# Kernel tuning notes

Measured on AMD Instinct MI355X. Metric: run time of the kernel, lower is better.

The kernel has to match this reference:

```python
import jax, jax.numpy as jnp
import numpy as np

B, S, D, H = 2, 2048, 1024, 16
DH = D // H
DFF = 4 * D
EPS = 1e-5


def layernorm(x, g, b):
    mu = jnp.mean(x, axis=-1, keepdims=True)
    var = jnp.mean(jnp.square(x - mu), axis=-1, keepdims=True)
    return (x - mu) * jax.lax.rsqrt(var + EPS) * g + b


def setup_inputs() -> dict:
    key = jax.random.key(0)
    ks = jax.random.split(key, 12)
    s = 0.02
    return {
        "x": jax.random.normal(ks[0], (B, S, D), dtype=jnp.float32),
        "ln1_g": jnp.ones((D,), jnp.float32),
        "ln1_b": jnp.zeros((D,), jnp.float32),
        "Wq": jax.random.normal(ks[1], (D, D), jnp.float32) * s,
        "bq": jnp.zeros((D,), jnp.float32),
        "Wk": jax.random.normal(ks[2], (D, D), jnp.float32) * s,
        "bk": jnp.zeros((D,), jnp.float32),
        "Wv": jax.random.normal(ks[3], (D, D), jnp.float32) * s,
        "bv": jnp.zeros((D,), jnp.float32),
        "Wo": jax.random.normal(ks[4], (D, D), jnp.float32) * s,
        "bo": jnp.zeros((D,), jnp.float32),
        "ln2_g": jnp.ones((D,), jnp.float32),
        "ln2_b": jnp.zeros((D,), jnp.float32),
        "W1": jax.random.normal(ks[5], (D, DFF), jnp.float32) * s,
        "b1": jnp.zeros((DFF,), jnp.float32),
        "W2": jax.random.normal(ks[6], (DFF, D), jnp.float32) * s,
        "b2": jnp.zeros((D,), jnp.float32),
    }


def block(x, ln1_g, ln1_b, Wq, bq, Wk, bk, Wv, bv, Wo, bo, ln2_g, ln2_b, W1, b1, W2, b2):
    h = layernorm(x, ln1_g, ln1_b)
    # projections -> [B, H, S, DH]
    q = (h @ Wq + bq).reshape(B, S, H, DH).transpose(0, 2, 1, 3)
    k = (h @ Wk + bk).reshape(B, S, H, DH).transpose(0, 2, 1, 3)
    v = (h @ Wv + bv).reshape(B, S, H, DH).transpose(0, 2, 1, 3)
    scores = jnp.einsum('bhqd,bhkd->bhqk', q, k) / jnp.sqrt(jnp.float32(DH))
    causal = jnp.tril(jnp.ones((S, S), dtype=bool))  # True = keep
    scores = jnp.where(causal, scores, -jnp.inf)
    attn = jax.nn.softmax(scores, axis=-1)
    out = jnp.einsum('bhqk,bhkd->bhqd', attn, v)
    out = out.transpose(0, 2, 1, 3).reshape(B, S, D)
    x = x + out @ Wo + bo
    h2 = layernorm(x, ln2_g, ln2_b)
    ff = jax.nn.gelu(h2 @ W1 + b1, approximate=False) @ W2 + b2
    return x + ff


def reference(x, ln1_g, ln1_b, Wq, bq, Wk, bk, Wv, bv, Wo, bo, ln2_g, ln2_b, W1, b1, W2, b2):
    return block(x, ln1_g, ln1_b, Wq, bq, Wk, bk, Wv, bv, Wo, bo, ln2_g, ln2_b, W1, b1, W2, b2)
```

## Files before the change

### kernel.cpp

```cpp
#include <hip/hip_runtime.h>
#include <cstdint>
#include <cstddef>


#define DEV static __device__ __forceinline__

typedef unsigned short u16;
typedef __bf16 bf16x8 __attribute__((ext_vector_type(8)));
typedef u16    u16x8  __attribute__((ext_vector_type(8)));
typedef u16    u16x4  __attribute__((ext_vector_type(4)));
typedef float  f32x4  __attribute__((ext_vector_type(4)));

#define AEXP2(x) __builtin_amdgcn_exp2f(x)

DEV u16 f2bf(float f) {
  unsigned u = __builtin_bit_cast(unsigned, f);
  u += 0x7fffu + ((u >> 16) & 1u);
  return (u16)(u >> 16);
}

DEV void gl16(const void* g, void* l) {
  __builtin_amdgcn_global_load_lds(
      (const __attribute__((address_space(1))) unsigned*)g,
      (__attribute__((address_space(3))) unsigned*)l, 16, 0, 0);
}

__global__ __launch_bounds__(256)
void tconv(const float* __restrict__ in, u16* __restrict__ out, int R, int C)
{
  __shared__ float tile[32][33];
  const int tx = threadIdx.x & 31, ty = threadIdx.x >> 5;
  const int r0 = blockIdx.y * 32, c0 = blockIdx.x * 32;
#pragma unroll
  for (int i = 0; i < 4; ++i)
    tile[ty + 8*i][tx] = in[(size_t)(r0 + ty + 8*i) * C + c0 + tx];
  __syncthreads();
#pragma unroll
  for (int i = 0; i < 4; ++i)
    out[(size_t)(c0 + ty + 8*i) * R + r0 + tx] = f2bf(tile[tx][ty + 8*i]);
}

__global__ __launch_bounds__(256)
void tconv4(const float* __restrict__ w0, const float* __restrict__ w1,
            const float* __restrict__ w2, const float* __restrict__ w3,
            u16* __restrict__ q0, u16* __restrict__ q1,
            u16* __restrict__ q2, u16* __restrict__ q3)
{
  __shared__ float tile[32][33];
  const int z = blockIdx.z;
  const float* in = z == 0 ? w0 : z == 1 ? w1 : z == 2 ? w2 : w3;
  u16* out       = z == 0 ? q0 : z == 1 ? q1 : z == 2 ? q2 : q3;
  const int tx = threadIdx.x & 31, ty = threadIdx.x >> 5;
  const int r0 = blockIdx.y * 32, c0 = blockIdx.x * 32;
#pragma unroll
  for (int i = 0; i < 4; ++i)
    tile[ty + 8*i][tx] = in[(size_t)(r0 + ty + 8*i) * 1024 + c0 + tx];
  __syncthreads();
#pragma unroll
  for (int i = 0; i < 4; ++i)
    out[(size_t)(c0 + ty + 8*i) * 1024 + r0 + tx] = f2bf(tile[tx][ty + 8*i]);
}

__global__ __launch_bounds__(256)
void ln_fwd(const float* __restrict__ x, const float* __restrict__ g,
            const float* __restrict__ b, u16* __restrict__ out)
{
  const int row = blockIdx.x, t = threadIdx.x;
  const float4 v = ((const float4*)(x + (size_t)row * 1024))[t];
  float s1 = v.x + v.y + v.z + v.w;
  float s2 = v.x*v.x + v.y*v.y + v.z*v.z + v.w*v.w;
#pragma unroll
  for (int d = 1; d < 64; d <<= 1) {
    s1 += __shfl_xor(s1, d, 64);
    s2 += __shfl_xor(s2, d, 64);
  }
  __shared__ float sh[8];
  const int w = t >> 6;
  if ((t & 63) == 0) { sh[w] = s1; sh[w + 4] = s2; }
  __syncthreads();
  s1 = sh[0] + sh[1] + sh[2] + sh[3];
  s2 = sh[4] + sh[5] + sh[6] + sh[7];
  const float mu  = s1 * (1.0f / 1024.0f);
  const float var = s2 * (1.0f / 1024.0f) - mu * mu;
  const float rs  = rsqrtf(var + 1e-5f);
  const float4 gv = ((const float4*)g)[t];
  const float4 bv = ((const float4*)b)[t];
  u16x4 o;
  o[0] = f2bf((v.x - mu) * rs * gv.x + bv.x);
  o[1] = f2bf((v.y - mu) * rs * gv.y + bv.y);
  o[2] = f2bf((v.z - mu) * rs * gv.z + bv.z);
  o[3] = f2bf((v.w - mu) * rs * gv.w + bv.w);
  *(u16x4*)(out + (size_t)row * 1024 + t * 4) = o;
}

#define EPI_QKV  0
#define EPI_RES  1
#define EPI_GELU 2

#define QSCALE 0.180421f

template<int EPI, int BM>
__global__ __launch_bounds__(256)
void gemm_bt(const u16* __restrict__ A, const u16* __restrict__ Bt,
             const float* __restrict__ b0, const float* __restrict__ b1,
             const float* __restrict__ b2, const float* __restrict__ res,
             float* __restrict__ outf, u16* __restrict__ o0,
             u16* __restrict__ o1, u16* __restrict__ o2,
             int N, int K)
{
  constexpr int MI = BM / 32;
  constexpr int RA = BM / 32;
  __shared__ u16 As[BM * 64];
  __shared__ u16 Bs[128 * 64];
  const int t = threadIdx.x, lane = t & 63, w = t >> 6;
  const int wr = w >> 1, wc = w & 1;
  const int m0 = blockIdx.y * BM, n0 = blockIdx.x * 128;
  const int li = lane & 15, lg = lane >> 4;

  const int srow = t >> 3;
  const int schunk = (t & 7) ^ (srow & 7);
  const u16* Ag = A  + (size_t)(m0 + srow) * K + schunk * 8;
  const u16* Bg = Bt + (size_t)(n0 + srow) * K + schunk * 8;

  f32x4 acc[MI][4] = {};

  for (int k0 = 0; k0 < K; k0 += 64) {
    __syncthreads();
#pragma unroll
    for (int p = 0; p < RA; ++p)
      gl16(Ag + k0 + (size_t)(p * 32) * K, &As[t * 8 + p * 2048]);
#pragma unroll
    for (int p = 0; p < 4; ++p)
      gl16(Bg + k0 + (size_t)(p * 32) * K, &Bs[t * 8 + p * 2048]);
    __syncthreads();
    const int swz = (li & 7) << 4;
#pragma unroll
    for (int ks = 0; ks < 2; ++ks) {
      bf16x8 af[MI], bfr[4];
#pragma unroll
      for (int i = 0; i < MI; ++i) {
        const int Ra = wr * (MI * 16) + i * 16 + li;
        af[i] = *(const bf16x8*)((const char*)As + Ra * 128 +
                                 ((ks * 64 + lg * 16) ^ swz));
      }
#pragma unroll
      for (int i = 0; i < 4; ++i) {
        const int Rb = wc * 64 + i * 16 + li;
        bfr[i] = *(const bf16x8*)((const char*)Bs + Rb * 128 +
                                  ((ks * 64 + lg * 16) ^ swz));
      }
#pragma unroll
      for (int mi = 0; mi < MI; ++mi)
#pragma unroll
        for (int ni = 0; ni < 4; ++ni)
          acc[mi][ni] = __builtin_amdgcn_mfma_f32_16x16x32_bf16(
              af[mi], bfr[ni], acc[mi][ni], 0, 0, 0);
    }
  }

  const int crow = wr * (MI * 16) + lg * 4;
  const int ccol = wc * 64 + li;

  if (EPI == EPI_QKV) {
    const int which = n0 >> 10;
    const float* bias = which == 0 ? b0 : which == 1 ? b1 : b2;
    const int nn0 = n0 & 1023;
    if (which == 2) {
#pragma unroll
      for (int mi = 0; mi < MI; ++mi)
#pragma unroll
        for (int ni = 0; ni < 4; ++ni) {
          const int gm0 = m0 + crow + mi * 16;
          const int b_ = gm0 >> 11, s_ = gm0 & 2047;
          const int gc = nn0 + ccol + ni * 16;
          const int h_ = gc >> 6, d_ = gc & 63;
          u16x4 pk;
#pragma unroll
          for (int r = 0; r < 4; ++r) pk[r] = f2bf(acc[mi][ni][r] + bias[gc]);
          *(u16x4*)(o2 + ((size_t)(b_ * 16 + h_) * 64 + d_) * 2048 + s_) = pk;
        }
    } else {
      u16* outp = which == 0 ? o0 : o1;
      const float sc = which == 0 ? QSCALE : 1.0f;
#pragma unroll
      for (int mi = 0; mi < MI; ++mi)
#pragma unroll
        for (int ni = 0; ni < 4; ++ni)
#pragma unroll
          for (int r = 0; r < 4; ++r) {
            const int gm = m0 + crow + mi * 16 + r;
            const int gc = nn0 + ccol + ni * 16;
            const float v = (acc[mi][ni][r] + bias[gc]) * sc;
            const int b_ = gm >> 11, s_ = gm & 2047;
            const int h_ = gc >> 6,  d_ = gc & 63;
            outp[((size_t)(b_ * 16 + h_) * 2048 + s_) * 64 + d_] = f2bf(v);
          }
    }
  } else {
#pragma unroll
    for (int mi = 0; mi < MI; ++mi)
#pragma unroll
      for (int ni = 0; ni < 4; ++ni)
#pragma unroll
        for (int r = 0; r < 4; ++r) {
          const int gm = m0 + crow + mi * 16 + r;
          const int gn = n0 + ccol + ni * 16;
          const float v = acc[mi][ni][r] + b0[gn];
          if (EPI == EPI_RES) {
            const size_t o = (size_t)gm * N + gn;
            outf[o] = v + res[o];
          } else {
            const float y = 0.7978845608f * (v + 0.044715f * v * v * v);
            const float e = AEXP2(fminf(y * 2.8853900818f, 80.0f));
            const float gl = v * e * __builtin_amdgcn_rcpf(e + 1.0f);
            o0[(size_t)gm * N + gn] = f2bf(gl);
          }
        }
  }
}

__global__ __launch_bounds__(512, 4)
void attn_fwd(const u16* __restrict__ qb, const u16* __restrict__ kb,
              const u16* __restrict__ vtb, u16* __restrict__ ob)
{
  __shared__ u16 Ks[2][128 * 64];
  __shared__ u16 Vt[2][64 * 128];
  __shared__ u16 Ps[8][16 * 64];
  const int t = threadIdx.x, w = t >> 6, lane = t & 63;
  const int li = lane & 15, lg = lane >> 4;
  const int bh = blockIdx.y;
  const int bx = blockIdx.x;
  const int qt = (bh & 16) ? (15 - bx) : bx;
  const int q0 = qt * 128;

  const size_t qrow = (size_t)bh * 2048 + q0 + w * 16 + li;
  const bf16x8 aq0 = *(const bf16x8*)(qb + qrow * 64 + lg * 8);
  const bf16x8 aq1 = *(const bf16x8*)(qb + qrow * 64 + lg * 8 + 32);

  f32x4 o[4] = {};
  float mrun[4], lrun[4];
#pragma unroll
  for (int r = 0; r < 4; ++r) { mrun[r] = -1e30f; lrun[r] = 0.0f; }

  const u16* kbase = kb  + (size_t)bh * 2048 * 64;
  const u16* vbase = vtb + (size_t)bh * 64 * 2048;
  const int ntile = qt + 1;

  const int kchunk = (t & 7)  ^ ((t >> 3) & 7);
  const int vchunk = (t & 15) ^ ((t >> 4) & 15);
  const u16* kg = kbase + (size_t)(t >> 3) * 64 + kchunk * 8;
  const u16* vg = vbase + (size_t)(t >> 4) * 2048 + vchunk * 8;

#define STAGE(tk_, b_)                                              \
  {                                                                 \
    const int kv0s = (tk_) * 128;                                   \
    gl16(kg + (size_t)kv0s * 64,        &Ks[b_][t * 8]);            \
    gl16(kg + (size_t)(kv0s + 64) * 64, &Ks[b_][t * 8 + 4096]);     \
    gl16(vg + kv0s,                     &Vt[b_][t * 8]);            \
    gl16(vg + kv0s + (size_t)32 * 2048, &Vt[b_][t * 8 + 4096]);     \
  }

  STAGE(0, 0);
  __syncthreads();

  for (int tk = 0; tk < ntile; ++tk) {
    const int cur = tk & 1;
    const int kv0 = tk * 128;
    if (tk + 1 < ntile) STAGE(tk + 1, 1 - cur);

    f32x4 s[8];
    __builtin_amdgcn_s_setprio(1);
#pragma unroll
    for (int cf = 0; cf < 8; ++cf) {
      const int row = cf * 16 + li;
      const char* kc = (const char*)Ks[cur] + row * 128;
      const int sw = (row & 7) << 4;
      const bf16x8 bk0 = *(const bf16x8*)(kc + ((lg * 16)      ^ sw));
      const bf16x8 bk1 = *(const bf16x8*)(kc + ((lg * 16 + 64) ^ sw));
      f32x4 z = {};
      z = __builtin_amdgcn_mfma_f32_16x16x32_bf16(aq0, bk0, z, 0, 0, 0);
      z = __builtin_amdgcn_mfma_f32_16x16x32_bf16(aq1, bk1, z, 0, 0, 0);
      s[cf] = z;
    }
    __builtin_amdgcn_s_setprio(0);
    const int row0 = q0 + w * 16 + lg * 4;
    if (tk == ntile - 1) {
#pragma unroll
      for (int cf = 0; cf < 8; ++cf)
#pragma unroll
        for (int r = 0; r < 4; ++r)
          if (kv0 + cf * 16 + li > row0 + r) s[cf][r] = -1e30f;
    }

    float pmax[4];
#pragma unroll
    for (int r = 0; r < 4; ++r) {
      float mx = s[0][r];
#pragma unroll
      for (int cf = 1; cf < 8; ++cf) mx = fmaxf(mx, s[cf][r]);
      pmax[r] = mx;
    }
#pragma unroll
    for (int d = 1; d < 16; d <<= 1)
#pragma unroll
      for (int r = 0; r < 4; ++r)
        pmax[r] = fmaxf(pmax[r], __shfl_xor(pmax[r], d, 64));

    bool need = false;
#pragma unroll
    for (int r = 0; r < 4; ++r) need = need || (pmax[r] > mrun[r] + 11.5f);
    if (__any((int)need)) {
#pragma unroll
      for (int r = 0; r < 4; ++r) {
        const float mnew = fmaxf(mrun[r], pmax[r]);
        const float scl  = AEXP2(mrun[r] - mnew);
        lrun[r] *= scl;
#pragma unroll
        for (int n = 0; n < 4; ++n) o[n][r] *= scl;
        mrun[r] = mnew;
      }
    }
    float ps[4] = {0.f, 0.f, 0.f, 0.f};
#pragma unroll
    for (int cf = 0; cf < 8; ++cf)
#pragma unroll
      for (int r = 0; r < 4; ++r) {
        const float pv = AEXP2(s[cf][r] - mrun[r]);
        s[cf][r] = pv;
        ps[r] += pv;
      }
#pragma unroll
    for (int d = 1; d < 16; d <<= 1)
#pragma unroll
      for (int r = 0; r < 4; ++r)
        ps[r] += __shfl_xor(ps[r], d, 64);
#pragma unroll
    for (int r = 0; r < 4; ++r) lrun[r] += ps[r];

#pragma unroll
    for (int kh = 0; kh < 2; ++kh) {
#pragma unroll
      for (int cf2 = 0; cf2 < 4; ++cf2)
#pragma unroll
        for (int r = 0; r < 4; ++r) {
          const int prow = lg * 4 + r;
          const int pcolB = (cf2 * 16 + li) * 2;
          *(u16*)((char*)Ps[w] + prow * 128 + (pcolB ^ ((prow & 7) << 4))) =
              f2bf(s[kh * 4 + cf2][r]);
        }
      __builtin_amdgcn_s_setprio(1);
#pragma unroll
      for (int ks = 0; ks < 2; ++ks) {
        const char* pc = (const char*)Ps[w] + li * 128;
        const bf16x8 ap =
            *(const bf16x8*)(pc + ((lg * 16 + ks * 64) ^ ((li & 7) << 4)));
#pragma unroll
        for (int n = 0; n < 4; ++n) {
          const int vrow = n * 16 + li;
          const char* vc = (const char*)Vt[cur] + vrow * 256;
          const int colB = lg * 16 + ks * 64 + kh * 128;
          const bf16x8 bv =
              *(const bf16x8*)(vc + (colB ^ ((vrow & 15) << 4)));
          o[n] = __builtin_amdgcn_mfma_f32_16x16x32_bf16(ap, bv, o[n], 0, 0, 0);
        }
      }
      __builtin_amdgcn_s_setprio(0);
    }

    __syncthreads();
  }
#undef STAGE

  float inv[4];
#pragma unroll
  for (int r = 0; r < 4; ++r) inv[r] = __builtin_amdgcn_rcpf(lrun[r]);
  const int b_ = bh >> 4, h_ = bh & 15;
#pragma unroll
  for (int n = 0; n < 4; ++n)
#pragma unroll
    for (int r = 0; r < 4; ++r) {
      const int rowg = q0 + w * 16 + lg * 4 + r;
      ob[((size_t)b_ * 2048 + rowg) * 1024 + h_ * 64 + n * 16 + li] =
          f2bf(o[n][r] * inv[r]);
    }
}

extern "C" void kernel_launch(void* const* d_in, const int* in_sizes, int n_in,
                              void* d_out, int out_size, void* d_ws, size_t ws_size,
                              hipStream_t stream) {
  const float* x    = (const float*)d_in[0];
  const float* ln1g = (const float*)d_in[1];
  const float* ln1b = (const float*)d_in[2];
  const float* Wq   = (const float*)d_in[3];
  const float* bq   = (const float*)d_in[4];
  const float* Wk   = (const float*)d_in[5];
  const float* bk   = (const float*)d_in[6];
  const float* Wv   = (const float*)d_in[7];
  const float* bv   = (const float*)d_in[8];
  const float* Wo   = (const float*)d_in[9];
  const float* bo   = (const float*)d_in[10];
  const float* ln2g = (const float*)d_in[11];
  const float* ln2b = (const float*)d_in[12];
  const float* W1   = (const float*)d_in[13];
  const float* b1   = (const float*)d_in[14];
  const float* W2   = (const float*)d_in[15];
  const float* b2   = (const float*)d_in[16];

  char* ws = (char*)d_ws;
  const size_t MB = 1u << 20;
  u16*   hb   = (u16*)(ws + 0);
  u16*   Wqt  = (u16*)(ws + 8  * MB);
  u16*   Wkt  = (u16*)(ws + 10 * MB);
  u16*   Wvt  = (u16*)(ws + 12 * MB);
  u16*   Wot  = (u16*)(ws + 14 * MB);
  u16*   W1t  = (u16*)(ws + 16 * MB);
  u16*   W2t  = (u16*)(ws + 24 * MB);
  u16*   qbuf = (u16*)(ws + 32 * MB);
  u16*   kbuf = (u16*)(ws + 40 * MB);
  u16*   aob  = (u16*)(ws + 48 * MB);
  u16*   vtb  = (u16*)(ws + 56 * MB);
  float* x2   = (float*)(ws + 64 * MB);
  u16*   h2   = hb;
  u16*   ff1  = qbuf;

  const dim3 blk(256);
  tconv4<<<dim3(32, 32, 4), blk, 0, stream>>>(Wq, Wk, Wv, Wo, Wqt, Wkt, Wvt, Wot);
  tconv<<<dim3(128, 32), blk, 0, stream>>>(W1, W1t, 1024, 4096);
  tconv<<<dim3(32, 128), blk, 0, stream>>>(W2, W2t, 4096, 1024);

  ln_fwd<<<4096, blk, 0, stream>>>(x, ln1g, ln1b, hb);

  gemm_bt<EPI_QKV, 128><<<dim3(24, 32), blk, 0, stream>>>(
      hb, Wqt, bq, bk, bv, nullptr, nullptr, qbuf, kbuf, vtb, 3072, 1024);

  attn_fwd<<<dim3(16, 32), dim3(512), 0, stream>>>(qbuf, kbuf, vtb, aob);

  gemm_bt<EPI_RES, 64><<<dim3(8, 64), blk, 0, stream>>>(
      aob, Wot, bo, nullptr, nullptr, x, x2, nullptr, nullptr, nullptr, 1024, 1024);

  ln_fwd<<<4096, blk, 0, stream>>>(x2, ln2g, ln2b, h2);

  gemm_bt<EPI_GELU, 128><<<dim3(32, 32), blk, 0, stream>>>(
      h2, W1t, b1, nullptr, nullptr, nullptr, nullptr, ff1, nullptr, nullptr, 4096, 1024);

  gemm_bt<EPI_RES, 64><<<dim3(8, 64), blk, 0, stream>>>(
      ff1, W2t, b2, nullptr, nullptr, x2, (float*)d_out, nullptr, nullptr, nullptr, 1024, 4096);
}
```

Measured before the change: 248.8 us.

## Add LDS double buffering and XCD-aware block remapping to GEMM kernel

Adds an optional double-buffered LDS pipeline to the bf16 GEMM, so the next K-tile is loaded with global_load_lds while MFMAs run on the current one. The double buffer is used for the two BM=64 residual GEMMs. All GEMMs also get a block-index remap that groups M tiles by d&7, roughly matching the round-robin dispatch of blocks across the 8 XCDs, so that each XCD's L2 sees more A/B reuse. The cost is double the LDS for the double-buffered variants, and the remap assumes the grid divides evenly by 8*CM.

```diff
diff --git a/kernel.cpp b/kernel.cpp
--- a/kernel.cpp
+++ b/kernel.cpp
@@ -99,7 +99,7 @@
 
 #define QSCALE 0.180421f
 
-template<int EPI, int BM>
+template<int EPI, int BM, bool DBUF, int CM>
 __global__ __launch_bounds__(256)
 void gemm_bt(const u16* __restrict__ A, const u16* __restrict__ Bt,
              const float* __restrict__ b0, const float* __restrict__ b1,
@@ -110,11 +110,15 @@
 {
   constexpr int MI = BM / 32;
   constexpr int RA = BM / 32;
-  __shared__ u16 As[BM * 64];
-  __shared__ u16 Bs[128 * 64];
+  constexpr int NB = DBUF ? 2 : 1;
+  __shared__ u16 As[NB][BM * 64];
+  __shared__ u16 Bs[NB][128 * 64];
   const int t = threadIdx.x, lane = t & 63, w = t >> 6;
   const int wr = w >> 1, wc = w & 1;
-  const int m0 = blockIdx.y * BM, n0 = blockIdx.x * 128;
+  const int d = blockIdx.x + gridDim.x * blockIdx.y;
+  const int rr = d >> 3;
+  const int m0 = ((d & 7) * CM + rr % CM) * BM;
+  const int n0 = (rr / CM) * 128;
   const int li = lane & 15, lg = lane >> 4;
 
   const int srow = t >> 3;
@@ -122,17 +126,30 @@
   const u16* Ag = A  + (size_t)(m0 + srow) * K + schunk * 8;
   const u16* Bg = Bt + (size_t)(n0 + srow) * K + schunk * 8;
 
+  auto STG = [&](int k0, int b) {
+#pragma unroll
+    for (int p = 0; p < RA; ++p)
+      gl16(Ag + k0 + (size_t)(p * 32) * K, &As[b][t * 8 + p * 2048]);
+#pragma unroll
+    for (int p = 0; p < 4; ++p)
+      gl16(Bg + k0 + (size_t)(p * 32) * K, &Bs[b][t * 8 + p * 2048]);
+  };
+
   f32x4 acc[MI][4] = {};
 
+  if (DBUF) { STG(0, 0); __syncthreads(); }
+
   for (int k0 = 0; k0 < K; k0 += 64) {
-    __syncthreads();
-#pragma unroll
-    for (int p = 0; p < RA; ++p)
-      gl16(Ag + k0 + (size_t)(p * 32) * K, &As[t * 8 + p * 2048]);
-#pragma unroll
-    for (int p = 0; p < 4; ++p)
-      gl16(Bg + k0 + (size_t)(p * 32) * K, &Bs[t * 8 + p * 2048]);
-    __syncthreads();
+    int cur;
+    if (DBUF) {
+      cur = (k0 >> 6) & 1;
+      if (k0 + 64 < K) STG(k0 + 64, 1 - cur);
+    } else {
+      cur = 0;
+      __syncthreads();
+      STG(k0, 0);
+      __syncthreads();
+    }
     const int swz = (li & 7) << 4;
 #pragma unroll
     for (int ks = 0; ks < 2; ++ks) {
@@ -140,13 +157,13 @@
 #pragma unroll
       for (int i = 0; i < MI; ++i) {
         const int Ra = wr * (MI * 16) + i * 16 + li;
-        af[i] = *(const bf16x8*)((const char*)As + Ra * 128 +
+        af[i] = *(const bf16x8*)((const char*)As[cur] + Ra * 128 +
                                  ((ks * 64 + lg * 16) ^ swz));
       }
 #pragma unroll
       for (int i = 0; i < 4; ++i) {
         const int Rb = wc * 64 + i * 16 + li;
-        bfr[i] = *(const bf16x8*)((const char*)Bs + Rb * 128 +
+        bfr[i] = *(const bf16x8*)((const char*)Bs[cur] + Rb * 128 +
                                   ((ks * 64 + lg * 16) ^ swz));
       }
 #pragma unroll
@@ -156,6 +173,7 @@
           acc[mi][ni] = __builtin_amdgcn_mfma_f32_16x16x32_bf16(
               af[mi], bfr[ni], acc[mi][ni], 0, 0, 0);
     }
+    if (DBUF) __syncthreads();
   }
 
   const int crow = wr * (MI * 16) + lg * 4;
@@ -430,19 +448,19 @@
 
   ln_fwd<<<4096, blk, 0, stream>>>(x, ln1g, ln1b, hb);
 
-  gemm_bt<EPI_QKV, 128><<<dim3(24, 32), blk, 0, stream>>>(
+  gemm_bt<EPI_QKV, 128, false, 4><<<dim3(24, 32), blk, 0, stream>>>(
       hb, Wqt, bq, bk, bv, nullptr, nullptr, qbuf, kbuf, vtb, 3072, 1024);
 
   attn_fwd<<<dim3(16, 32), dim3(512), 0, stream>>>(qbuf, kbuf, vtb, aob);
 
-  gemm_bt<EPI_RES, 64><<<dim3(8, 64), blk, 0, stream>>>(
+  gemm_bt<EPI_RES, 64, true, 8><<<dim3(8, 64), blk, 0, stream>>>(
       aob, Wot, bo, nullptr, nullptr, x, x2, nullptr, nullptr, nullptr, 1024, 1024);
 
   ln_fwd<<<4096, blk, 0, stream>>>(x2, ln2g, ln2b, h2);
 
-  gemm_bt<EPI_GELU, 128><<<dim3(32, 32), blk, 0, stream>>>(
+  gemm_bt<EPI_GELU, 128, false, 4><<<dim3(32, 32), blk, 0, stream>>>(
       h2, W1t, b1, nullptr, nullptr, nullptr, nullptr, ff1, nullptr, nullptr, 4096, 1024);
 
-  gemm_bt<EPI_RES, 64><<<dim3(8, 64), blk, 0, stream>>>(
+  gemm_bt<EPI_RES, 64, true, 8><<<dim3(8, 64), blk, 0, stream>>>(
       ff1, W2t, b2, nullptr, nullptr, x2, (float*)d_out, nullptr, nullptr, nullptr, 1024, 4096);
 }
```

New measurement: 241.1 us. 1.03x faster.
